# Optimization experiments

Measured on AMD Instinct MI355X. Metric: run time of the kernel, lower is better.

## Reference

```python
import jax, jax.numpy as jnp
import numpy as np

B, N, D, H, M = 4, 1024, 768, 12, 100
HD = D // H
FF = 4 * D


def layer_norm(x, g, b, eps=1e-5):
    mu = x.mean(-1, keepdims=True)
    var = ((x - mu) ** 2).mean(-1, keepdims=True)
    return (x - mu) / jnp.sqrt(var + eps) * g + b


def _rel_pos_logits(q_pos, rel_emb):
    """Fairseq LearnedRelativePositionalEmbedding (unmasked, per-head).
    q_pos: (B, N, H, HD). Faithful to the torch call: flat reshape to (N, B*H, HD).
    Returns absolute-indexed positional logits of shape (B*H, N, N)."""
    b, l, h, d = q_pos.shape
    query = q_pos.reshape(l, b * h, d)  # flat reshape exactly as in torch code
    pad_len = max(l - M, 0)
    start = max(M - l, 0)
    emb = rel_emb[..., 0]  # (H, 2M-1, HD)
    emb = jnp.pad(emb, ((0, 0), (pad_len, pad_len), (0, 0)))
    emb = jax.lax.dynamic_slice_in_dim(emb, start, 2 * l - 1, axis=1)
    emb = jax.lax.stop_gradient(emb)  # torch wraps the pad in no_grad
    qv = query.reshape(l, -1, h, d)  # (l, B, H, HD)
    pl = jnp.einsum('lbhd,hmd->lbhm', qv, emb).reshape(l, -1, 2 * l - 1)
    if pad_len > 0:  # mask relative positions beyond max_relative_pos
        mask = np.zeros((2 * l - 1,), np.float32)
        mask[:pad_len] = -1e8
        mask[2 * l - 1 - pad_len:] = -1e8
        pl = pl + jnp.asarray(mask)
    # relative -> absolute indexing (unmasked skewing trick)
    xp = jnp.pad(pl, ((0, 0), (0, 0), (0, 1)))          # (l, BH, 2l)
    xp = xp.transpose(1, 0, 2).reshape(b * h, l * 2 * l)
    xp = jnp.pad(xp, ((0, 0), (0, l - 1)))
    xp = xp.reshape(b * h, l + 1, 2 * l - 1)
    return xp[:, :l, l - 1:]                             # (BH, l, l)


def setup_inputs() -> dict:
    key = jax.random.key(0)
    ks = jax.random.split(key, 8)
    p = lambda k, shape: jax.random.normal(k, shape, dtype=jnp.float32) * 0.02
    return {
        'src': jax.random.normal(ks[0], (B, N, D), dtype=jnp.float32),
        'qkv_w': p(ks[1], (3 * D, D)),
        'qkv_b': jnp.zeros((3 * D,), jnp.float32),
        'rel_emb': jax.random.normal(ks[2], (H, 2 * M - 1, HD, 1), dtype=jnp.float32) * (HD ** -0.5),
        'proj_w': p(ks[3], (D, D)),
        'proj_b': jnp.zeros((D,), jnp.float32),
        'ln1_g': jnp.ones((D,), jnp.float32),
        'ln1_b': jnp.zeros((D,), jnp.float32),
        'fc1_w': p(ks[4], (FF, D)),
        'fc1_b': jnp.zeros((FF,), jnp.float32),
        'fc2_w': p(ks[5], (D, FF)),
        'fc2_b': jnp.zeros((D,), jnp.float32),
        'ln2_g': jnp.ones((D,), jnp.float32),
        'ln2_b': jnp.zeros((D,), jnp.float32),
    }


def reference(src, qkv_w, qkv_b, rel_emb, proj_w, proj_b, ln1_g, ln1_b,
              fc1_w, fc1_b, fc2_w, fc2_b, ln2_g, ln2_b):
    b, n, dmod = src.shape
    qkv = (src @ qkv_w.T + qkv_b).reshape(b, n, 3, H, HD).transpose(2, 0, 3, 1, 4)
    q, k, v = qkv[0], qkv[1], qkv[2]  # (B, H, N, HD)
    logits = jnp.einsum('bhnd,bhmd->bhnm', q, k) * (1.0 / np.sqrt(HD))
    pos = _rel_pos_logits(q.transpose(0, 2, 1, 3), rel_emb).reshape(b, H, n, n)
    probs = jax.nn.softmax(logits + pos, axis=-1)  # dropout is identity at eval / p=0
    out = jnp.einsum('bhnm,bhmd->bhnd', probs, v).transpose(0, 2, 1, 3).reshape(b, n, dmod)
    attn_out = out @ proj_w.T + proj_b
    x = layer_norm(src + attn_out, ln1_g, ln1_b)
    h1 = jax.nn.gelu(x @ fc1_w.T + fc1_b, approximate=False)
    x = layer_norm(x + h1 @ fc2_w.T + fc2_b, ln2_g, ln2_b)
    return x
```

## Files before the change

kernel.cpp:

```cpp
#include <hip/hip_runtime.h>
#include <hip/hip_bf16.h>
#include <math.h>


typedef __attribute__((ext_vector_type(8))) short bf16x8;
typedef __attribute__((ext_vector_type(4))) float f32x4;

#define GLDS16(g, l) __builtin_amdgcn_global_load_lds( \
    (const __attribute__((address_space(1))) void*)(g), \
    (__attribute__((address_space(3))) void*)(l), 16, 0, 0)

__device__ __forceinline__ unsigned short f2bu(float x) {
    union { __hip_bfloat16 h; unsigned short u; } c;
    c.h = __float2bfloat16(x);
    return c.u;
}
__device__ __forceinline__ float bu2f(unsigned short u) {
    union { __hip_bfloat16 h; unsigned short u; } c;
    c.u = u;
    return __bfloat162float(c.h);
}

__global__ void __launch_bounds__(256)
convert_all_kernel(const float* __restrict__ s0, const float* __restrict__ s1,
                   const float* __restrict__ s2, const float* __restrict__ s3,
                   const float* __restrict__ s4,
                   unsigned short* __restrict__ d0, unsigned short* __restrict__ d1,
                   unsigned short* __restrict__ d2, unsigned short* __restrict__ d3,
                   unsigned short* __restrict__ d4)
{
    const int idx = blockIdx.x * 256 + threadIdx.x;
    const float* s; unsigned short* d; int off;
    if (idx < 786432)       { s = s0; d = d0; off = idx; }
    else if (idx < 1228800) { s = s1; d = d1; off = idx - 786432; }
    else if (idx < 1376256) { s = s2; d = d2; off = idx - 1228800; }
    else if (idx < 1966080) { s = s3; d = d3; off = idx - 1376256; }
    else if (idx < 2555904) { s = s4; d = d4; off = idx - 1966080; }
    else return;
    const float4 v = ((const float4*)s)[off];
    ushort4 o;
    o.x = f2bu(v.x); o.y = f2bu(v.y); o.z = f2bu(v.z); o.w = f2bu(v.w);
    ((ushort4*)d)[off] = o;
}

__global__ void __launch_bounds__(256)
embpad_kernel(const float* __restrict__ rel, unsigned short* __restrict__ embpad)
{
    const int idx = blockIdx.x * 256 + threadIdx.x;
    if (idx >= 12 * 256 * 64) return;
    const int d = idx & 63;
    const int rp = (idx >> 6) & 255;
    const int h = idx >> 14;
    embpad[idx] = (rp < 199) ? f2bu(rel[((h * 199 + rp) << 6) + d]) : (unsigned short)0;
}

#define SWZ_OFF(ch, row7) ((((ch) ^ (row7)) * 8))

template<int MODE>
__global__ void __launch_bounds__(256)
gemm64_kernel(const unsigned short* __restrict__ A, const unsigned short* __restrict__ Wt,
              const float* __restrict__ bias, unsigned short* __restrict__ Cb,
              int Ndim, int K, int Ksplit,
              unsigned short* __restrict__ qb, unsigned short* __restrict__ kb,
              unsigned short* __restrict__ vTb)
{
    __shared__ short As[2 * 128 * 64];
    __shared__ short Bs[2 * 64 * 64];
    const int tid = threadIdx.x;
    const int l = tid & 63;
    const int w = tid >> 6;
    const int wr = w >> 1, wc = w & 1;

    int flat = blockIdx.y * gridDim.x + blockIdx.x;
    const int nxy = gridDim.x * gridDim.y;
    flat = (flat & 7) * (nxy >> 3) + (flat >> 3);
    const int bx = flat % gridDim.x;
    const int by = flat / gridDim.x;

    const int row0 = by * 128;
    const int col0 = bx * 64;
    const int koff = blockIdx.z * Ksplit;
    const int nt = Ksplit >> 6;

    const int lrow = l >> 3;
    const int lcol = ((l & 7) ^ lrow) * 8;
    const int l7 = l & 7;

    f32x4 acc[4][2];
#pragma unroll
    for (int m = 0; m < 4; ++m)
#pragma unroll
        for (int n = 0; n < 2; ++n) acc[m][n] = (f32x4){0.f, 0.f, 0.f, 0.f};

#define STAGE(buf, t) do {                                                        \
    const int k0 = koff + (t) * 64;                                               \
    _Pragma("unroll")                                                             \
    for (int it = 0; it < 4; ++it) {                                              \
        const int c = w * 4 + it;                                                 \
        GLDS16(A + (size_t)(row0 + c * 8 + lrow) * K + k0 + lcol,                 \
               As + (buf) * 8192 + c * 512);                                      \
    }                                                                             \
    _Pragma("unroll")                                                             \
    for (int it = 0; it < 2; ++it) {                                              \
        const int c = w * 2 + it;                                                 \
        GLDS16(Wt + (size_t)(col0 + c * 8 + lrow) * K + k0 + lcol,                \
               Bs + (buf) * 4096 + c * 512);                                      \
    }                                                                             \
} while (0)

    STAGE(0, 0);
    __syncthreads();

    for (int t = 0; t < nt; ++t) {
        const int buf = t & 1;
        if (t + 1 < nt) STAGE(buf ^ 1, t + 1);
        const short* a = As + buf * 8192;
        const short* bsp = Bs + buf * 4096;
#pragma unroll
        for (int kk = 0; kk < 2; ++kk) {
            const int ch = kk * 4 + (l >> 4);
            bf16x8 af[4], bfr[2];
#pragma unroll
            for (int m = 0; m < 4; ++m)
                af[m] = *(const bf16x8*)(a + (wr * 64 + m * 16 + (l & 15)) * 64 + SWZ_OFF(ch, l7));
#pragma unroll
            for (int n = 0; n < 2; ++n)
                bfr[n] = *(const bf16x8*)(bsp + (wc * 32 + n * 16 + (l & 15)) * 64 + SWZ_OFF(ch, l7));
#pragma unroll
            for (int m = 0; m < 4; ++m)
#pragma unroll
                for (int n = 0; n < 2; ++n)
                    acc[m][n] = __builtin_amdgcn_mfma_f32_16x16x32_bf16(af[m], bfr[n], acc[m][n], 0, 0, 0);
        }
        if (t + 1 < nt) __syncthreads();
    }
#undef STAGE

#pragma unroll
    for (int m = 0; m < 4; ++m) {
#pragma unroll
        for (int n = 0; n < 2; ++n) {
#pragma unroll
            for (int r = 0; r < 4; ++r) {
                const int row = row0 + wr * 64 + m * 16 + (l >> 4) * 4 + r;
                const int col = col0 + wc * 32 + n * 16 + (l & 15);
                if (MODE == 0) {
                    const float v = acc[m][n][r] + bias[col];
                    const int which = col / 768;
                    const int rem = col - which * 768;
                    const int h = rem >> 6, d = rem & 63;
                    const int b = row >> 10, nn = row & 1023;
                    if (which == 0)
                        qb[((size_t)(b * 12 + h) * 1024 + nn) * 64 + d] = f2bu(v);
                    else if (which == 1)
                        kb[((size_t)(b * 12 + h) * 1024 + nn) * 64 + d] = f2bu(v);
                    else
                        vTb[((size_t)(b * 12 + h) * 64 + d) * 1024 + nn] = f2bu(v);
                } else if (MODE == 2) {
                    const float v = acc[m][n][r] + bias[col];
                    const float u = 0.7978845608028654f * (v + 0.044715f * v * v * v);
                    const float th = 1.0f - 2.0f / (__expf(2.0f * u) + 1.0f);
                    Cb[(size_t)row * Ndim + col] = f2bu(0.5f * v * (1.0f + th));
                } else {
                    unsigned short* dst = Cb + (size_t)blockIdx.z * 4096 * Ndim;
                    dst[(size_t)row * Ndim + col] = f2bu(acc[m][n][r]);
                }
            }
        }
    }
}

__global__ void __launch_bounds__(256)
attn_mfma_kernel(const unsigned short* __restrict__ qb, const unsigned short* __restrict__ kb,
                 const unsigned short* __restrict__ vTb, const unsigned short* __restrict__ embpad,
                 unsigned short* __restrict__ ctx)
{
    __shared__ __attribute__((aligned(16))) char lds[58368];
    short* Qps = (short*)(lds);
    short* Qs = (short*)(lds);
    short* Stage = (short*)(lds + 8192);
    unsigned short* Spos = (unsigned short*)(lds + 24576);
    short* PLall = (short*)(lds);
    short* Vt = (short*)(lds + 40960);

    const int i0 = blockIdx.x * 64;
    const int h = blockIdx.y, b = blockIdx.z;
    const int tid = threadIdx.x;
    const int l = tid & 63, w = tid >> 6;
    const int lm = l & 15, lg4 = l >> 4;
    const int l7 = l & 7;
    const int lrow = l >> 3;
    const int lcolsw = ((l & 7) ^ lrow) * 8;
    const size_t bh = (size_t)(b * 12 + h);

#pragma unroll
    for (int c = 0; c < 2; ++c) {
        const int row = w * 16 + c * 8 + lrow;
        const int iq = i0 + row;
        const int t2 = iq * 4 + b;
        const int b2 = t2 >> 10, n2 = t2 & 1023;
        const unsigned short* g = qb + ((size_t)(b2 * 12 + h) * 1024 + n2) * 64 + lcolsw;
        GLDS16(g, Qps + (w * 16 + c * 8) * 64);
    }
    __syncthreads();

    bf16x8 afp[2];
#pragma unroll
    for (int kk = 0; kk < 2; ++kk)
        afp[kk] = *(const bf16x8*)(Qps + (w * 16 + lm) * 64 + SWZ_OFF(kk * 4 + lg4, l7));

#pragma unroll
    for (int et = 0; et < 4; ++et) {
        __syncthreads();
#pragma unroll
        for (int c = 0; c < 2; ++c) {
            const int row = w * 16 + c * 8 + lrow;
            const unsigned short* g = embpad + ((size_t)h * 256 + et * 64 + row) * 64 + lcolsw;
            GLDS16(g, Stage + (w * 16 + c * 8) * 64);
        }
        __syncthreads();
        f32x4 cp[4];
#pragma unroll
        for (int sub = 0; sub < 4; ++sub) cp[sub] = (f32x4){0.f, 0.f, 0.f, 0.f};
#pragma unroll
        for (int kk = 0; kk < 2; ++kk)
#pragma unroll
            for (int sub = 0; sub < 4; ++sub) {
                const bf16x8 bv = *(const bf16x8*)(Stage + (sub * 16 + lm) * 64 + SWZ_OFF(kk * 4 + lg4, l7));
                cp[sub] = __builtin_amdgcn_mfma_f32_16x16x32_bf16(afp[kk], bv, cp[sub], 0, 0, 0);
            }
#pragma unroll
        for (int sub = 0; sub < 4; ++sub)
#pragma unroll
            for (int r = 0; r < 4; ++r)
                Spos[(w * 16 + lg4 * 4 + r) * 264 + et * 64 + sub * 16 + lm] = f2bu(cp[sub][r]);
    }

#pragma unroll
    for (int c = 0; c < 2; ++c) {
        const int row = w * 16 + c * 8 + lrow;
        const unsigned short* g = qb + (bh * 1024 + i0 + row) * 64 + lcolsw;
        GLDS16(g, Qs + (w * 16 + c * 8) * 64);
    }

    const int jw0 = (i0 > 128) ? i0 - 128 : 0;
    const int hiex = (i0 + 163 < 1024) ? i0 + 163 : 1024;
    const int nt = (hiex - jw0 + 63) >> 6;

    f32x4 s[5][4];
#pragma unroll
    for (int ct = 0; ct < 5; ++ct)
#pragma unroll
        for (int sub = 0; sub < 4; ++sub) s[ct][sub] = (f32x4){0.f, 0.f, 0.f, 0.f};
    bf16x8 afq[2];

#pragma unroll
    for (int ct = 0; ct < 5; ++ct) {
        __syncthreads();
        if (ct < nt) {
#pragma unroll
            for (int c = 0; c < 2; ++c) {
                const int row = w * 16 + c * 8 + lrow;
                const unsigned short* g = kb + (bh * 1024 + jw0 + ct * 64 + row) * 64 + lcolsw;
                GLDS16(g, Stage + (w * 16 + c * 8) * 64);
            }
        }
        __syncthreads();
        if (ct == 0) {
#pragma unroll
            for (int kk = 0; kk < 2; ++kk)
                afq[kk] = *(const bf16x8*)(Qs + (w * 16 + lm) * 64 + SWZ_OFF(kk * 4 + lg4, l7));
        }
        if (ct < nt) {
#pragma unroll
            for (int kk = 0; kk < 2; ++kk)
#pragma unroll
                for (int sub = 0; sub < 4; ++sub) {
                    const bf16x8 bv = *(const bf16x8*)(Stage + (sub * 16 + lm) * 64 + SWZ_OFF(kk * 4 + lg4, l7));
                    s[ct][sub] = __builtin_amdgcn_mfma_f32_16x16x32_bf16(afq[kk], bv, s[ct][sub], 0, 0, 0);
                }
        }
    }

    const int irel = w * 16 + lg4 * 4;
    float mx[4] = {-1e30f, -1e30f, -1e30f, -1e30f};
#pragma unroll
    for (int ct = 0; ct < 5; ++ct)
#pragma unroll
        for (int sub = 0; sub < 4; ++sub)
#pragma unroll
            for (int r = 0; r < 4; ++r) {
                const int i = i0 + irel + r;
                const int j = jw0 + ct * 64 + sub * 16 + lm;
                const int rr = j - i + 99;
                const int rc = (rr < 0) ? 0 : (rr > 198 ? 198 : rr);
                const float ps = bu2f(Spos[(irel + r) * 264 + rc]);
                const bool ok = (ct < nt) && (rr >= 0) && (rr <= 198);
                const float lg = ok ? (0.125f * s[ct][sub][r] + ps) : -1e30f;
                s[ct][sub][r] = lg;
                mx[r] = fmaxf(mx[r], lg);
            }
#pragma unroll
    for (int m = 1; m < 16; m <<= 1)
#pragma unroll
        for (int r = 0; r < 4; ++r) mx[r] = fmaxf(mx[r], __shfl_xor(mx[r], m, 64));

    float sm[4] = {0.f, 0.f, 0.f, 0.f};
#pragma unroll
    for (int ct = 0; ct < 5; ++ct)
#pragma unroll
        for (int sub = 0; sub < 4; ++sub)
#pragma unroll
            for (int r = 0; r < 4; ++r) {
                const float p = __expf(s[ct][sub][r] - mx[r]);
                s[ct][sub][r] = p;
                sm[r] += p;
            }
#pragma unroll
    for (int m = 1; m < 16; m <<= 1)
#pragma unroll
        for (int r = 0; r < 4; ++r) sm[r] += __shfl_xor(sm[r], m, 64);
    float inv[4];
#pragma unroll
    for (int r = 0; r < 4; ++r) inv[r] = 1.0f / sm[r];

    __syncthreads();

    short* PLw = PLall + w * 5120;
#pragma unroll
    for (int ct = 0; ct < 5; ++ct)
#pragma unroll
        for (int sub = 0; sub < 4; ++sub)
#pragma unroll
            for (int r = 0; r < 4; ++r) {
                const int rowrel = lg4 * 4 + r;
                const int colrel = ct * 64 + sub * 16 + lm;
                int byte = rowrel * 640 + colrel * 2;
                byte ^= ((rowrel & 7) << 4);
                *(short*)((char*)PLw + byte) = (short)f2bu(s[ct][sub][r] * inv[r]);
            }

    f32x4 o[4];
#pragma unroll
    for (int sub = 0; sub < 4; ++sub) o[sub] = (f32x4){0.f, 0.f, 0.f, 0.f};
#pragma unroll
    for (int ct = 0; ct < 5; ++ct) {
        if (ct < nt) {
#pragma unroll
            for (int c = 0; c < 2; ++c) {
                const int dd = w * 16 + c * 8 + lrow;
                const unsigned short* g = vTb + (bh * 64 + dd) * 1024 + jw0 + ct * 64 + lcolsw;
                GLDS16(g, Vt + (w * 16 + c * 8) * 64);
            }
        }
        __syncthreads();
        if (ct < nt) {
#pragma unroll
            for (int kk = 0; kk < 2; ++kk) {
                const int colrel = ct * 64 + kk * 32 + lg4 * 8;
                int byte = lm * 640 + colrel * 2;
                byte ^= ((lm & 7) << 4);
                const bf16x8 ap = *(const bf16x8*)((char*)PLw + byte);
#pragma unroll
                for (int sub = 0; sub < 4; ++sub) {
                    const bf16x8 bv = *(const bf16x8*)(Vt + (sub * 16 + lm) * 64 + SWZ_OFF(kk * 4 + lg4, l7));
                    o[sub] = __builtin_amdgcn_mfma_f32_16x16x32_bf16(ap, bv, o[sub], 0, 0, 0);
                }
            }
        }
        __syncthreads();
    }

#pragma unroll
    for (int sub = 0; sub < 4; ++sub)
#pragma unroll
        for (int r = 0; r < 4; ++r) {
            const int i = i0 + w * 16 + lg4 * 4 + r;
            const int d = sub * 16 + lm;
            ctx[((size_t)b * 1024 + i) * 768 + h * 64 + d] = f2bu(o[sub][r]);
        }
}

__global__ void __launch_bounds__(256)
ln_fuse_kernel(const unsigned short* __restrict__ p0, const unsigned short* __restrict__ p1,
               const float* __restrict__ bias,
               const float* __restrict__ residf, const unsigned short* __restrict__ residb,
               const float* __restrict__ g, const float* __restrict__ bta,
               float* __restrict__ outf, unsigned short* __restrict__ outb)
{
    const int row = blockIdx.x;
    const int t = threadIdx.x;
    const size_t base = (size_t)row * 768;
    float v[3];
#pragma unroll
    for (int e = 0; e < 3; ++e) {
        const int idx = t + e * 256;
        const float r = residf ? residf[base + idx] : bu2f(residb[base + idx]);
        v[e] = bu2f(p0[base + idx]) + bu2f(p1[base + idx]) + bias[idx] + r;
    }
    __shared__ float red[4];
    float s = v[0] + v[1] + v[2];
#pragma unroll
    for (int off = 32; off > 0; off >>= 1) s += __shfl_down(s, off);
    if ((t & 63) == 0) red[t >> 6] = s;
    __syncthreads();
    const float mu = (red[0] + red[1] + red[2] + red[3]) * (1.0f / 768.0f);
    __syncthreads();
    const float d0 = v[0] - mu, d1 = v[1] - mu, d2 = v[2] - mu;
    float q = d0 * d0 + d1 * d1 + d2 * d2;
#pragma unroll
    for (int off = 32; off > 0; off >>= 1) q += __shfl_down(q, off);
    if ((t & 63) == 0) red[t >> 6] = q;
    __syncthreads();
    const float var = (red[0] + red[1] + red[2] + red[3]) * (1.0f / 768.0f);
    const float rstd = rsqrtf(var + 1e-5f);
    const float y0 = d0 * rstd * g[t] + bta[t];
    const float y1 = d1 * rstd * g[t + 256] + bta[t + 256];
    const float y2 = d2 * rstd * g[t + 512] + bta[t + 512];
    if (outf) { outf[base + t] = y0; outf[base + t + 256] = y1; outf[base + t + 512] = y2; }
    if (outb) { outb[base + t] = f2bu(y0); outb[base + t + 256] = f2bu(y1); outb[base + t + 512] = f2bu(y2); }
}

extern "C" void kernel_launch(void* const* d_in, const int* in_sizes, int n_in,
                              void* d_out, int out_size, void* d_ws, size_t ws_size,
                              hipStream_t stream)
{
    const float* src    = (const float*)d_in[0];
    const float* qkv_w  = (const float*)d_in[1];
    const float* qkv_b  = (const float*)d_in[2];
    const float* rel    = (const float*)d_in[3];
    const float* proj_w = (const float*)d_in[4];
    const float* proj_b = (const float*)d_in[5];
    const float* ln1_g  = (const float*)d_in[6];
    const float* ln1_b  = (const float*)d_in[7];
    const float* fc1_w  = (const float*)d_in[8];
    const float* fc1_b  = (const float*)d_in[9];
    const float* fc2_w  = (const float*)d_in[10];
    const float* fc2_b  = (const float*)d_in[11];
    const float* ln2_g  = (const float*)d_in[12];
    const float* ln2_b  = (const float*)d_in[13];
    float* out = (float*)d_out;
    char* W = (char*)d_ws;

    unsigned short* q_b     = (unsigned short*)(W + 0);
    unsigned short* k_b     = (unsigned short*)(W + 6291456);
    unsigned short* vT_b    = (unsigned short*)(W + 12582912);
    unsigned short* src_b   = (unsigned short*)(W + 18874368);
    unsigned short* ctx_b   = (unsigned short*)(W + 18874368);
    unsigned short* h1_b    = (unsigned short*)(W + 0);
    unsigned short* qkvw_b  = (unsigned short*)(W + 25165824);
    unsigned short* PP      = (unsigned short*)(W + 25165824);
    unsigned short* FP      = (unsigned short*)(W + 25165824);
    unsigned short* projw_b = (unsigned short*)(W + 37748736);
    unsigned short* fc1w_b  = (unsigned short*)(W + 38928384);
    unsigned short* fc2w_b  = (unsigned short*)(W + 43646976);
    unsigned short* embp_b  = (unsigned short*)(W + 48365568);
    unsigned short* xbuf_b  = (unsigned short*)(W + 48758784);

    convert_all_kernel<<<9984, 256, 0, stream>>>(
        src, qkv_w, proj_w, fc1_w, fc2_w, src_b, qkvw_b, projw_b, fc1w_b, fc2w_b);
    embpad_kernel<<<768, 256, 0, stream>>>(rel, embp_b);

    gemm64_kernel<0><<<dim3(36, 32, 1), 256, 0, stream>>>(
        src_b, qkvw_b, qkv_b, nullptr, 2304, 768, 768, q_b, k_b, vT_b);

    attn_mfma_kernel<<<dim3(16, 12, 4), 256, 0, stream>>>(q_b, k_b, vT_b, embp_b, ctx_b);

    gemm64_kernel<3><<<dim3(12, 32, 2), 256, 0, stream>>>(
        ctx_b, projw_b, nullptr, PP, 768, 768, 384, nullptr, nullptr, nullptr);

    ln_fuse_kernel<<<4096, 256, 0, stream>>>(
        PP, PP + 4096 * 768, proj_b, src, nullptr, ln1_g, ln1_b, nullptr, xbuf_b);

    gemm64_kernel<2><<<dim3(48, 32, 1), 256, 0, stream>>>(
        xbuf_b, fc1w_b, fc1_b, h1_b, 3072, 768, 768, nullptr, nullptr, nullptr);

    gemm64_kernel<3><<<dim3(12, 32, 2), 256, 0, stream>>>(
        h1_b, fc2w_b, nullptr, FP, 768, 3072, 1536, nullptr, nullptr, nullptr);

    ln_fuse_kernel<<<4096, 256, 0, stream>>>(
        FP, FP + 4096 * 768, fc2_b, nullptr, xbuf_b, ln2_g, ln2_b, out, nullptr);
}
```

Before: 171.1 us.

## Widen GEMM tiles to 128x128 and drop LDS double buffering

The GEMM kernel's output tile grows from 128x64 to 128x128 columns, so each wave computes a 64x64 block (4x4 MFMA fragments) and operand reuse per LDS load increases. The double-buffered async staging is replaced by a single buffer loaded between two barriers each K step, which keeps LDS usage about the same. Each launch now has half as many blocks. The trade-off is that global loads no longer overlap the MFMA work, and grids such as the split-K projection (6x32x2=384 blocks) may underfill the 256 CUs.

```diff
diff --git a/kernel.cpp b/kernel.cpp
--- a/kernel.cpp
+++ b/kernel.cpp
@@ -58,14 +58,14 @@
 
 template<int MODE>
 __global__ void __launch_bounds__(256)
-gemm64_kernel(const unsigned short* __restrict__ A, const unsigned short* __restrict__ Wt,
-              const float* __restrict__ bias, unsigned short* __restrict__ Cb,
-              int Ndim, int K, int Ksplit,
-              unsigned short* __restrict__ qb, unsigned short* __restrict__ kb,
-              unsigned short* __restrict__ vTb)
-{
-    __shared__ short As[2 * 128 * 64];
-    __shared__ short Bs[2 * 64 * 64];
+gemm128_kernel(const unsigned short* __restrict__ A, const unsigned short* __restrict__ Wt,
+               const float* __restrict__ bias, unsigned short* __restrict__ Cb,
+               int Ndim, int K, int Ksplit,
+               unsigned short* __restrict__ qb, unsigned short* __restrict__ kb,
+               unsigned short* __restrict__ vTb)
+{
+    __shared__ short As[128 * 64];
+    __shared__ short Bs[128 * 64];
     const int tid = threadIdx.x;
     const int l = tid & 63;
     const int w = tid >> 6;
@@ -78,72 +78,57 @@
     const int by = flat / gridDim.x;
 
     const int row0 = by * 128;
-    const int col0 = bx * 64;
+    const int col0 = bx * 128;
     const int koff = blockIdx.z * Ksplit;
     const int nt = Ksplit >> 6;
 
     const int lrow = l >> 3;
     const int lcol = ((l & 7) ^ lrow) * 8;
     const int l7 = l & 7;
-
-    f32x4 acc[4][2];
+    const int lm = l & 15, lg4 = l >> 4;
+
+    f32x4 acc[4][4];
 #pragma unroll
     for (int m = 0; m < 4; ++m)
 #pragma unroll
-        for (int n = 0; n < 2; ++n) acc[m][n] = (f32x4){0.f, 0.f, 0.f, 0.f};
-
-#define STAGE(buf, t) do {                                                        \
-    const int k0 = koff + (t) * 64;                                               \
-    _Pragma("unroll")                                                             \
-    for (int it = 0; it < 4; ++it) {                                              \
-        const int c = w * 4 + it;                                                 \
-        GLDS16(A + (size_t)(row0 + c * 8 + lrow) * K + k0 + lcol,                 \
-               As + (buf) * 8192 + c * 512);                                      \
-    }                                                                             \
-    _Pragma("unroll")                                                             \
-    for (int it = 0; it < 2; ++it) {                                              \
-        const int c = w * 2 + it;                                                 \
-        GLDS16(Wt + (size_t)(col0 + c * 8 + lrow) * K + k0 + lcol,                \
-               Bs + (buf) * 4096 + c * 512);                                      \
-    }                                                                             \
-} while (0)
-
-    STAGE(0, 0);
-    __syncthreads();
+        for (int n = 0; n < 4; ++n) acc[m][n] = (f32x4){0.f, 0.f, 0.f, 0.f};
 
     for (int t = 0; t < nt; ++t) {
-        const int buf = t & 1;
-        if (t + 1 < nt) STAGE(buf ^ 1, t + 1);
-        const short* a = As + buf * 8192;
-        const short* bsp = Bs + buf * 4096;
+        const int k0 = koff + t * 64;
+        __syncthreads();
+#pragma unroll
+        for (int it = 0; it < 4; ++it) {
+            const int c = w * 4 + it;
+            GLDS16(A + (size_t)(row0 + c * 8 + lrow) * K + k0 + lcol, As + c * 512);
+            GLDS16(Wt + (size_t)(col0 + c * 8 + lrow) * K + k0 + lcol, Bs + c * 512);
+        }
+        __syncthreads();
 #pragma unroll
         for (int kk = 0; kk < 2; ++kk) {
-            const int ch = kk * 4 + (l >> 4);
-            bf16x8 af[4], bfr[2];
+            const int ch = kk * 4 + lg4;
+            bf16x8 af[4], bfr[4];
 #pragma unroll
             for (int m = 0; m < 4; ++m)
-                af[m] = *(const bf16x8*)(a + (wr * 64 + m * 16 + (l & 15)) * 64 + SWZ_OFF(ch, l7));
-#pragma unroll
-            for (int n = 0; n < 2; ++n)
-                bfr[n] = *(const bf16x8*)(bsp + (wc * 32 + n * 16 + (l & 15)) * 64 + SWZ_OFF(ch, l7));
+                af[m] = *(const bf16x8*)(As + (wr * 64 + m * 16 + lm) * 64 + SWZ_OFF(ch, l7));
+#pragma unroll
+            for (int n = 0; n < 4; ++n)
+                bfr[n] = *(const bf16x8*)(Bs + (wc * 64 + n * 16 + lm) * 64 + SWZ_OFF(ch, l7));
 #pragma unroll
             for (int m = 0; m < 4; ++m)
 #pragma unroll
-                for (int n = 0; n < 2; ++n)
+                for (int n = 0; n < 4; ++n)
                     acc[m][n] = __builtin_amdgcn_mfma_f32_16x16x32_bf16(af[m], bfr[n], acc[m][n], 0, 0, 0);
         }
-        if (t + 1 < nt) __syncthreads();
-    }
-#undef STAGE
+    }
 
 #pragma unroll
     for (int m = 0; m < 4; ++m) {
 #pragma unroll
-        for (int n = 0; n < 2; ++n) {
+        for (int n = 0; n < 4; ++n) {
 #pragma unroll
             for (int r = 0; r < 4; ++r) {
-                const int row = row0 + wr * 64 + m * 16 + (l >> 4) * 4 + r;
-                const int col = col0 + wc * 32 + n * 16 + (l & 15);
+                const int row = row0 + wr * 64 + m * 16 + lg4 * 4 + r;
+                const int col = col0 + wc * 64 + n * 16 + lm;
                 if (MODE == 0) {
                     const float v = acc[m][n][r] + bias[col];
                     const int which = col / 768;
@@ -461,21 +446,21 @@
         src, qkv_w, proj_w, fc1_w, fc2_w, src_b, qkvw_b, projw_b, fc1w_b, fc2w_b);
     embpad_kernel<<<768, 256, 0, stream>>>(rel, embp_b);
 
-    gemm64_kernel<0><<<dim3(36, 32, 1), 256, 0, stream>>>(
+    gemm128_kernel<0><<<dim3(18, 32, 1), 256, 0, stream>>>(
         src_b, qkvw_b, qkv_b, nullptr, 2304, 768, 768, q_b, k_b, vT_b);
 
     attn_mfma_kernel<<<dim3(16, 12, 4), 256, 0, stream>>>(q_b, k_b, vT_b, embp_b, ctx_b);
 
-    gemm64_kernel<3><<<dim3(12, 32, 2), 256, 0, stream>>>(
+    gemm128_kernel<3><<<dim3(6, 32, 2), 256, 0, stream>>>(
         ctx_b, projw_b, nullptr, PP, 768, 768, 384, nullptr, nullptr, nullptr);
 
     ln_fuse_kernel<<<4096, 256, 0, stream>>>(
         PP, PP + 4096 * 768, proj_b, src, nullptr, ln1_g, ln1_b, nullptr, xbuf_b);
 
-    gemm64_kernel<2><<<dim3(48, 32, 1), 256, 0, stream>>>(
+    gemm128_kernel<2><<<dim3(24, 32, 1), 256, 0, stream>>>(
         xbuf_b, fc1w_b, fc1_b, h1_b, 3072, 768, 768, nullptr, nullptr, nullptr);
 
-    gemm64_kernel<3><<<dim3(12, 32, 2), 256, 0, stream>>>(
+    gemm128_kernel<3><<<dim3(6, 32, 2), 256, 0, stream>>>(
         h1_b, fc2w_b, nullptr, FP, 768, 3072, 1536, nullptr, nullptr, nullptr);
 
     ln_fuse_kernel<<<4096, 256, 0, stream>>>(
```

Result: slower. 188.9 us (+10.4%).
